# Kernel optimization log

Measured on AMD Instinct MI355X. Metric: run time of the kernel, lower is better.

Reference implementation:

```python
import jax, jax.numpy as jnp
import numpy as np

B, C_IN, C_INTER, H, W = 4, 256, 128, 64, 64


def _conv1x1(x, w, b):
    # x: [B,C,H,W], w: [O,C], b: [O] -> [B,O,H,W]
    return jnp.einsum('bchw,oc->bohw', x, w) + b[None, :, None, None]


def setup_inputs() -> dict:
    key = jax.random.key(0)
    ks = jax.random.split(key, 9)
    s_in = 1.0 / np.sqrt(C_IN)
    s_it = 1.0 / np.sqrt(C_INTER)
    return {
        'x': jax.random.normal(ks[0], (B, C_IN, H, W), dtype=jnp.float32),
        'theta_w': jax.random.normal(ks[1], (C_INTER, C_IN), dtype=jnp.float32) * s_in,
        'theta_b': jax.random.normal(ks[2], (C_INTER,), dtype=jnp.float32) * s_in,
        'phi_w': jax.random.normal(ks[3], (C_INTER, C_IN), dtype=jnp.float32) * s_in,
        'phi_b': jax.random.normal(ks[4], (C_INTER,), dtype=jnp.float32) * s_in,
        'g_w': jax.random.normal(ks[5], (C_INTER, C_IN), dtype=jnp.float32) * s_in,
        'g_b': jax.random.normal(ks[6], (C_INTER,), dtype=jnp.float32) * s_in,
        'W_w': jax.random.normal(ks[7], (C_IN, C_INTER), dtype=jnp.float32) * s_it,
        'W_b': jax.random.normal(ks[8], (C_IN,), dtype=jnp.float32) * s_it,
    }


def reference(x, theta_w, theta_b, phi_w, phi_b, g_w, g_b, W_w, W_b):
    b, c, h, w = x.shape
    n = h * w
    theta_x = _conv1x1(x, theta_w, theta_b).reshape(b, -1, n)  # [B,Ci,N]
    phi_x = _conv1x1(x, phi_w, phi_b).reshape(b, -1, n)        # [B,Ci,N]
    # f[b,i,j] = sum_c theta[b,c,i] * phi[b,c,j]  -> [B,N,N]
    f = jnp.einsum('bci,bcj->bij', theta_x, phi_x)
    # NOTE: softmax over dim=1 (the query/theta axis), as in the original code
    f_div_C = jax.nn.softmax(f, axis=1)
    g_x = _conv1x1(x, g_w, g_b).reshape(b, -1, n)              # [B,Ci,N]
    # y = f_div_C @ g_x^T, then permute back to [B,Ci,N] in one einsum
    y = jnp.einsum('bij,bcj->bci', f_div_C, g_x)
    y = y.reshape(b, -1, h, w)
    W_y = _conv1x1(y, W_w, W_b)
    return W_y + x
```

## Files before the change

kernel.cpp:

```cpp
#include <hip/hip_runtime.h>
#include <hip/hip_fp16.h>

#define NB   4
#define CIN  256
#define CM   128
#define NPIX 4096
#define LOG2E 1.44269504088896340736f

typedef _Float16 half_t;
typedef _Float16 f16x8 __attribute__((ext_vector_type(8)));
typedef _Float16 f16x4 __attribute__((ext_vector_type(4)));
typedef float    f32x4 __attribute__((ext_vector_type(4)));

static __device__ __forceinline__ f16x8 load8h(const half_t* p) {
    return *reinterpret_cast<const f16x8*>(p);
}
static __device__ __forceinline__ void gload_lds16(const void* g, void* l) {
    __builtin_amdgcn_global_load_lds(
        (const __attribute__((address_space(1))) unsigned int*)g,
        (__attribute__((address_space(3))) unsigned int*)l, 16, 0, 0);
}

__global__ __launch_bounds__(256) void k_pre(
    const float* __restrict__ tw, const float* __restrict__ pw,
    const float* __restrict__ gw, const float* __restrict__ Ww,
    half_t* __restrict__ TWh, half_t* __restrict__ PWh,
    half_t* __restrict__ GWh, half_t* __restrict__ WWh)
{
    const int m  = blockIdx.x >> 5;
    const int i4 = (blockIdx.x & 31) * 256 + threadIdx.x;
    const float* src = m == 0 ? tw : m == 1 ? pw : m == 2 ? gw : Ww;
    half_t*      dst = m == 0 ? TWh : m == 1 ? PWh : m == 2 ? GWh : WWh;
    float4 a = reinterpret_cast<const float4*>(src)[i4];
    f16x4 h = {(_Float16)a.x, (_Float16)a.y, (_Float16)a.z, (_Float16)a.w};
    *reinterpret_cast<f16x4*>(dst + (size_t)i4 * 4) = h;
}

__global__ __launch_bounds__(256) void k_proj(
    const float* __restrict__ x,
    const half_t* __restrict__ tw, const float* __restrict__ tb,
    const half_t* __restrict__ pw, const float* __restrict__ pb,
    const half_t* __restrict__ gw, const float* __restrict__ gb,
    half_t* __restrict__ T, half_t* __restrict__ P, half_t* __restrict__ G)
{
    __shared__ half_t xT[64][280];
    const int b  = blockIdx.x >> 6;
    const int p0 = (blockIdx.x & 63) << 6;
    const int tid = threadIdx.x;
    const int lane = tid & 63, wv = tid >> 6;
    const int r15 = lane & 15, g4 = lane >> 4;

    {
        const float* xb = x + (size_t)b * CIN * NPIX + p0;
        const int ii = tid & 63;
        const int k0 = tid >> 6;
        #pragma unroll 4
        for (int kk = 0; kk < 64; ++kk) {
            int k = kk * 4 + k0;
            xT[ii][k] = (half_t)xb[(size_t)k * NPIX + ii];
        }
    }
    __syncthreads();

    f16x8 afr[8];
    #pragma unroll
    for (int kg = 0; kg < 8; ++kg)
        afr[kg] = load8h(&xT[wv * 16 + r15][kg * 32 + g4 * 8]);

    #pragma unroll
    for (int p = 0; p < 2; ++p) {
        const half_t* wp = p ? pw : tw;
        const float*  bp = p ? pb : tb;
        half_t* OUT     = p ? P  : T;
        for (int cs = 0; cs < 8; ++cs) {
            f32x4 acc = {0.f, 0.f, 0.f, 0.f};
            const int crow = cs * 16 + r15;
            const half_t* wr = wp + (size_t)crow * CIN;
            #pragma unroll
            for (int kg = 0; kg < 8; ++kg) {
                f16x8 bf = load8h(wr + kg * 32 + g4 * 8);
                acc = __builtin_amdgcn_mfma_f32_16x16x32_f16(afr[kg], bf, acc, 0, 0, 0);
            }
            const float bias = bp[crow];
            #pragma unroll
            for (int r = 0; r < 4; ++r) {
                int pos = p0 + wv * 16 + g4 * 4 + r;
                OUT[((size_t)b * NPIX + pos) * CM + crow] = (half_t)(acc[r] + bias);
            }
        }
    }

    for (int cs = 0; cs < 8; ++cs) {
        f32x4 acc = {0.f, 0.f, 0.f, 0.f};
        const int crow = cs * 16 + r15;
        const half_t* wr = gw + (size_t)crow * CIN;
        #pragma unroll
        for (int kg = 0; kg < 8; ++kg) {
            f16x8 af = load8h(wr + kg * 32 + g4 * 8);
            acc = __builtin_amdgcn_mfma_f32_16x16x32_f16(af, afr[kg], acc, 0, 0, 0);
        }
        #pragma unroll
        for (int r = 0; r < 4; ++r) {
            int c = cs * 16 + g4 * 4 + r;
            int j = p0 + wv * 16 + r15;
            G[((size_t)b * CM + c) * NPIX + j] = (half_t)(acc[r] + gb[c]);
        }
    }
}

__global__ __launch_bounds__(512) void k_stats(
    const half_t* __restrict__ T, const half_t* __restrict__ P,
    float* __restrict__ M2, float* __restrict__ RD)
{
    __shared__ float partm[8][64];
    __shared__ float parts[8][64];
    const int b  = blockIdx.x >> 6;
    const int j0 = (blockIdx.x & 63) << 6;
    const int tid = threadIdx.x;
    const int lane = tid & 63, w = tid >> 6;
    const int r15 = lane & 15, g4 = lane >> 4;

    f16x8 bfr[4][4];
    const half_t* Pbase = P + (size_t)b * NPIX * CM;
    #pragma unroll
    for (int js = 0; js < 4; ++js)
        #pragma unroll
        for (int kg = 0; kg < 4; ++kg)
            bfr[js][kg] = load8h(Pbase + (size_t)(j0 + js * 16 + r15) * CM + kg * 32 + g4 * 8);

    float m2[4] = {-1e30f, -1e30f, -1e30f, -1e30f};
    float ss[4] = {0.f, 0.f, 0.f, 0.f};
    const half_t* Tb = T + (size_t)b * NPIX * CM;

    for (int it = 0; it < 8; ++it) {
        const int ibase = w * 512 + it * 64;
        #pragma unroll
        for (int is = 0; is < 4; ++is) {
            f16x8 af[4];
            const half_t* Tr = Tb + (size_t)(ibase + is * 16 + r15) * CM;
            #pragma unroll
            for (int kg = 0; kg < 4; ++kg) af[kg] = load8h(Tr + kg * 32 + g4 * 8);
            #pragma unroll
            for (int js = 0; js < 4; ++js) {
                f32x4 acc = {0.f, 0.f, 0.f, 0.f};
                #pragma unroll
                for (int kg = 0; kg < 4; ++kg)
                    acc = __builtin_amdgcn_mfma_f32_16x16x32_f16(af[kg], bfr[js][kg], acc, 0, 0, 0);
                float v0 = acc[0] * LOG2E, v1 = acc[1] * LOG2E;
                float v2 = acc[2] * LOG2E, v3 = acc[3] * LOG2E;
                float fm = fmaxf(fmaxf(v0, v1), fmaxf(v2, v3));
                float nm = fmaxf(m2[js], fm);
                ss[js] = ss[js] * exp2f(m2[js] - nm)
                       + (exp2f(v0 - nm) + exp2f(v1 - nm) + exp2f(v2 - nm) + exp2f(v3 - nm));
                m2[js] = nm;
            }
        }
    }
    #pragma unroll
    for (int js = 0; js < 4; ++js) {
        #pragma unroll
        for (int off = 16; off < 64; off <<= 1) {
            float om = __shfl_xor(m2[js], off);
            float os = __shfl_xor(ss[js], off);
            float nm = fmaxf(m2[js], om);
            ss[js] = ss[js] * exp2f(m2[js] - nm) + os * exp2f(om - nm);
            m2[js] = nm;
        }
        if (g4 == 0) { partm[w][js * 16 + r15] = m2[js]; parts[w][js * 16 + r15] = ss[js]; }
    }
    __syncthreads();
    if (tid < 64) {
        float m = -1e30f, s = 0.f;
        #pragma unroll
        for (int w2 = 0; w2 < 8; ++w2) {
            float om = partm[w2][tid], os = parts[w2][tid];
            float nm = fmaxf(m, om);
            s = s * exp2f(m - nm) + os * exp2f(om - nm);
            m = nm;
        }
        M2[b * NPIX + j0 + tid] = m;
        RD[b * NPIX + j0 + tid] = 1.0f / s;
    }
}

__global__ __launch_bounds__(256) void k_attn(
    const half_t* __restrict__ T, const half_t* __restrict__ P,
    const half_t* __restrict__ G,
    const float* __restrict__ M2, const float* __restrict__ RD,
    half_t* __restrict__ Y0, half_t* __restrict__ Y1)
{
    __shared__ half_t Pst[2][64 * 128];
    __shared__ half_t Gst[2][128 * 64];
    __shared__ half_t wlds[64][72];

    const int blk = blockIdx.x;
    const int b  = blk >> 7;
    const int ih = (blk >> 1) & 63;
    const int wg = blk & 1;
    const int i0 = ih << 6;
    const int tid = threadIdx.x;
    const int lane = tid & 63, wv = tid >> 6;
    const int r15 = lane & 15, g4 = lane >> 4;

    const half_t* Pb = P + (size_t)b * NPIX * CM;
    const half_t* Gb = G + (size_t)b * CM * NPIX;
    const float*  M2b = M2 + b * NPIX;
    const float*  RDb = RD + b * NPIX;

    f16x8 a1[4];
    const half_t* Tb = T + ((size_t)b * NPIX + i0 + wv * 16 + r15) * CM;
    #pragma unroll
    for (int kg = 0; kg < 4; ++kg) a1[kg] = load8h(Tb + kg * 32 + g4 * 8);

    f32x4 yacc[8];
    #pragma unroll
    for (int cs = 0; cs < 8; ++cs) yacc[cs] = (f32x4){0.f, 0.f, 0.f, 0.f};

    auto stageP = [&](int buf, int jb) {
        #pragma unroll
        for (int q = 0; q < 4; ++q) {
            int lo  = (wv * 4 + q) * 1024 + lane * 16;
            int row = lo >> 8;
            int cb  = lo & 255;
            const char* src = (const char*)Pb + (size_t)(jb + row) * (CM * 2)
                            + (cb ^ ((row & 7) << 4));
            gload_lds16(src, (char*)&Pst[buf][0] + (wv * 4 + q) * 1024);
        }
    };
    auto stageG = [&](int buf, int jb) {
        #pragma unroll
        for (int q = 0; q < 4; ++q) {
            int lo  = (wv * 4 + q) * 1024 + lane * 16;
            int row = lo >> 7;
            int cb  = lo & 127;
            const char* src = (const char*)Gb + (size_t)row * (NPIX * 2) + (size_t)jb * 2
                            + (cb ^ ((row & 7) << 4));
            gload_lds16(src, (char*)&Gst[buf][0] + (wv * 4 + q) * 1024);
        }
    };

    stageP(0, (wg * 32) * 64);
    stageG(0, (wg * 32) * 64);
    for (int jt = 0; jt < 32; ++jt) {
        const int jb = (wg * 32 + jt) * 64;
        const int cur = jt & 1;
        __syncthreads();
        if (jt < 31) { stageP(cur ^ 1, jb + 64); stageG(cur ^ 1, jb + 64); }

        const int swz = (r15 & 7) << 4;
        #pragma unroll
        for (int js = 0; js < 4; ++js) {
            f32x4 acc = {0.f, 0.f, 0.f, 0.f};
            const int row = js * 16 + r15;
            #pragma unroll
            for (int kg = 0; kg < 4; ++kg) {
                const char* pa = (const char*)&Pst[cur][0] + row * 256 + ((kg * 64 + g4 * 16) ^ swz);
                f16x8 bf = *reinterpret_cast<const f16x8*>(pa);
                acc = __builtin_amdgcn_mfma_f32_16x16x32_f16(a1[kg], bf, acc, 0, 0, 0);
            }
            const int j = jb + js * 16 + r15;
            const float mj = M2b[j], rdj = RDb[j];
            #pragma unroll
            for (int r = 0; r < 4; ++r) {
                float wgt = exp2f(fmaf(acc[r], LOG2E, -mj)) * rdj;
                wlds[wv * 16 + g4 * 4 + r][js * 16 + r15] = (half_t)wgt;
            }
        }

        f16x8 a2[2];
        #pragma unroll
        for (int kk = 0; kk < 2; ++kk)
            a2[kk] = load8h(&wlds[wv * 16 + r15][kk * 32 + g4 * 8]);
        #pragma unroll
        for (int cs = 0; cs < 8; ++cs) {
            const char* gbase = (const char*)&Gst[cur][0] + (cs * 16 + r15) * 128;
            #pragma unroll
            for (int kk = 0; kk < 2; ++kk) {
                f16x8 b2 = *reinterpret_cast<const f16x8*>(gbase + ((kk * 64 + g4 * 16) ^ swz));
                yacc[cs] = __builtin_amdgcn_mfma_f32_16x16x32_f16(a2[kk], b2, yacc[cs], 0, 0, 0);
            }
        }
    }

    half_t* Yp = wg ? Y1 : Y0;
    #pragma unroll
    for (int cs = 0; cs < 8; ++cs)
        #pragma unroll
        for (int r = 0; r < 4; ++r)
            Yp[((size_t)b * NPIX + i0 + wv * 16 + g4 * 4 + r) * CM + cs * 16 + r15]
                = (half_t)yacc[cs][r];
}

__global__ __launch_bounds__(256) void k_out(
    const half_t* __restrict__ Y0, const half_t* __restrict__ Y1,
    const half_t* __restrict__ Ww, const float* __restrict__ Wb,
    const float* __restrict__ x, float* __restrict__ out)
{
    const int b  = blockIdx.x >> 6;
    const int i0 = (blockIdx.x & 63) << 6;
    const int lane = threadIdx.x & 63, wv = threadIdx.x >> 6;
    const int r15 = lane & 15, g4 = lane >> 4;

    f16x8 yf[4];
    const size_t yrow = ((size_t)b * NPIX + i0 + wv * 16 + r15) * CM;
    #pragma unroll
    for (int kg = 0; kg < 4; ++kg) {
        f16x8 y0 = load8h(Y0 + yrow + kg * 32 + g4 * 8);
        f16x8 y1 = load8h(Y1 + yrow + kg * 32 + g4 * 8);
        yf[kg] = y0 + y1;
    }

    for (int os = 0; os < 16; ++os) {
        f32x4 acc = {0.f, 0.f, 0.f, 0.f};
        const half_t* wr = Ww + (size_t)(os * 16 + r15) * CM;
        #pragma unroll
        for (int kg = 0; kg < 4; ++kg) {
            f16x8 af = load8h(wr + kg * 32 + g4 * 8);
            acc = __builtin_amdgcn_mfma_f32_16x16x32_f16(af, yf[kg], acc, 0, 0, 0);
        }
        #pragma unroll
        for (int r = 0; r < 4; ++r) {
            int o = os * 16 + g4 * 4 + r;
            size_t addr = ((size_t)(b * CIN + o)) * NPIX + i0 + wv * 16 + r15;
            out[addr] = acc[r] + Wb[o] + x[addr];
        }
    }
}

extern "C" void kernel_launch(void* const* d_in, const int* in_sizes, int n_in,
                              void* d_out, int out_size, void* d_ws, size_t ws_size,
                              hipStream_t stream) {
    const float* x  = (const float*)d_in[0];
    const float* tw = (const float*)d_in[1];
    const float* tb = (const float*)d_in[2];
    const float* pw = (const float*)d_in[3];
    const float* pb = (const float*)d_in[4];
    const float* gw = (const float*)d_in[5];
    const float* gb = (const float*)d_in[6];
    const float* Ww = (const float*)d_in[7];
    const float* Wb = (const float*)d_in[8];
    float* out = (float*)d_out;

    const size_t SZ = (size_t)NB * NPIX * CM;
    const size_t WSZ = (size_t)CM * CIN;
    half_t* T   = (half_t*)d_ws;
    half_t* P   = T + SZ;
    half_t* G   = P + SZ;
    half_t* Y0  = G + SZ;
    half_t* Y1  = Y0 + SZ;
    half_t* TWh = Y1 + SZ;
    half_t* PWh = TWh + WSZ;
    half_t* GWh = PWh + WSZ;
    half_t* WWh = GWh + WSZ;
    float*  M2  = (float*)(WWh + WSZ);
    float*  RD  = M2 + (size_t)NB * NPIX;

    hipLaunchKernelGGL(k_pre,   dim3(128), dim3(256), 0, stream,
                       tw, pw, gw, Ww, TWh, PWh, GWh, WWh);
    hipLaunchKernelGGL(k_proj,  dim3(256), dim3(256), 0, stream,
                       x, TWh, tb, PWh, pb, GWh, gb, T, P, G);
    hipLaunchKernelGGL(k_stats, dim3(256), dim3(512), 0, stream, T, P, M2, RD);
    hipLaunchKernelGGL(k_attn,  dim3(512), dim3(256), 0, stream,
                       T, P, G, M2, RD, Y0, Y1);
    hipLaunchKernelGGL(k_out,   dim3(256), dim3(256), 0, stream,
                       Y0, Y1, WWh, Wb, x, out);
}
```

Before: 260.0 us.

## Split attention and stats work finer, drop weight LDS round-trip, fold softmax normalizer into logsumexp

Each k_stats block now covers 128 key columns and half of the query rows, writing partial max and sum values that a new k_merge kernel combines into one log-sum-exp per column. k_attn is split four ways along j (1024 blocks) and computes P·T with the operands swapped, so the exp weights land directly in the MFMA B-operand layout and feed 16x16x16 MFMAs without going through the wlds shared buffer. G is single-buffered with explicit vmcnt waits and a raw s_barrier, and the LSE values are loaded into LDS with an asynchronous 4-byte global-to-LDS load. The cost is four partial Y buffers to write and sum in k_out, an extra launch, and correctness that depends on hand-counted vmcnt values.

Result: slower. 271.6 us (+4.5%).

```diff
diff --git a/kernel.cpp b/kernel.cpp
--- a/kernel.cpp
+++ b/kernel.cpp
@@ -19,6 +19,11 @@
     __builtin_amdgcn_global_load_lds(
         (const __attribute__((address_space(1))) unsigned int*)g,
         (__attribute__((address_space(3))) unsigned int*)l, 16, 0, 0);
+}
+static __device__ __forceinline__ void gload_lds4(const void* g, void* l) {
+    __builtin_amdgcn_global_load_lds(
+        (const __attribute__((address_space(1))) unsigned int*)g,
+        (__attribute__((address_space(3))) unsigned int*)l, 4, 0, 0);
 }
 
 __global__ __launch_bounds__(256) void k_pre(
@@ -110,38 +115,41 @@
 
 __global__ __launch_bounds__(512) void k_stats(
     const half_t* __restrict__ T, const half_t* __restrict__ P,
-    float* __restrict__ M2, float* __restrict__ RD)
-{
-    __shared__ float partm[8][64];
-    __shared__ float parts[8][64];
+    float* __restrict__ Mp, float* __restrict__ Sp)
+{
+    __shared__ float partm[8][128];
+    __shared__ float parts[8][128];
     const int b  = blockIdx.x >> 6;
-    const int j0 = (blockIdx.x & 63) << 6;
+    const int jt = (blockIdx.x >> 1) & 31;
+    const int ih = blockIdx.x & 1;
+    const int j0 = jt * 128;
     const int tid = threadIdx.x;
     const int lane = tid & 63, w = tid >> 6;
     const int r15 = lane & 15, g4 = lane >> 4;
 
-    f16x8 bfr[4][4];
+    f16x8 bfr[8][4];
     const half_t* Pbase = P + (size_t)b * NPIX * CM;
     #pragma unroll
-    for (int js = 0; js < 4; ++js)
+    for (int js = 0; js < 8; ++js)
         #pragma unroll
         for (int kg = 0; kg < 4; ++kg)
             bfr[js][kg] = load8h(Pbase + (size_t)(j0 + js * 16 + r15) * CM + kg * 32 + g4 * 8);
 
-    float m2[4] = {-1e30f, -1e30f, -1e30f, -1e30f};
-    float ss[4] = {0.f, 0.f, 0.f, 0.f};
+    float m2[8], ss[8];
+    #pragma unroll
+    for (int js = 0; js < 8; ++js) { m2[js] = -1e30f; ss[js] = 0.f; }
     const half_t* Tb = T + (size_t)b * NPIX * CM;
-
-    for (int it = 0; it < 8; ++it) {
-        const int ibase = w * 512 + it * 64;
+    const int ibase0 = ih * 2048 + w * 256;
+
+    for (int it = 0; it < 4; ++it) {
         #pragma unroll
         for (int is = 0; is < 4; ++is) {
             f16x8 af[4];
-            const half_t* Tr = Tb + (size_t)(ibase + is * 16 + r15) * CM;
+            const half_t* Tr = Tb + (size_t)(ibase0 + it * 64 + is * 16 + r15) * CM;
             #pragma unroll
             for (int kg = 0; kg < 4; ++kg) af[kg] = load8h(Tr + kg * 32 + g4 * 8);
             #pragma unroll
-            for (int js = 0; js < 4; ++js) {
+            for (int js = 0; js < 8; ++js) {
                 f32x4 acc = {0.f, 0.f, 0.f, 0.f};
                 #pragma unroll
                 for (int kg = 0; kg < 4; ++kg)
@@ -157,7 +165,7 @@
         }
     }
     #pragma unroll
-    for (int js = 0; js < 4; ++js) {
+    for (int js = 0; js < 8; ++js) {
         #pragma unroll
         for (int off = 16; off < 64; off <<= 1) {
             float om = __shfl_xor(m2[js], off);
@@ -169,7 +177,7 @@
         if (g4 == 0) { partm[w][js * 16 + r15] = m2[js]; parts[w][js * 16 + r15] = ss[js]; }
     }
     __syncthreads();
-    if (tid < 64) {
+    if (tid < 128) {
         float m = -1e30f, s = 0.f;
         #pragma unroll
         for (int w2 = 0; w2 < 8; ++w2) {
@@ -178,34 +186,47 @@
             s = s * exp2f(m - nm) + os * exp2f(om - nm);
             m = nm;
         }
-        M2[b * NPIX + j0 + tid] = m;
-        RD[b * NPIX + j0 + tid] = 1.0f / s;
-    }
+        const size_t idx = (size_t)ih * (NB * NPIX) + b * NPIX + j0 + tid;
+        Mp[idx] = m;
+        Sp[idx] = s;
+    }
+}
+
+__global__ __launch_bounds__(256) void k_merge(
+    const float* __restrict__ Mp, const float* __restrict__ Sp,
+    float* __restrict__ C)
+{
+    const int idx = blockIdx.x * 256 + threadIdx.x;
+    const int nn = NB * NPIX;
+    float m0 = Mp[idx], m1 = Mp[nn + idx];
+    float s0 = Sp[idx], s1 = Sp[nn + idx];
+    float mm = fmaxf(m0, m1);
+    float s = s0 * exp2f(m0 - mm) + s1 * exp2f(m1 - mm);
+    C[idx] = mm + log2f(s);
 }
 
 __global__ __launch_bounds__(256) void k_attn(
     const half_t* __restrict__ T, const half_t* __restrict__ P,
-    const half_t* __restrict__ G,
-    const float* __restrict__ M2, const float* __restrict__ RD,
-    half_t* __restrict__ Y0, half_t* __restrict__ Y1)
+    const half_t* __restrict__ G, const float* __restrict__ C,
+    half_t* __restrict__ Y)
 {
     __shared__ half_t Pst[2][64 * 128];
-    __shared__ half_t Gst[2][128 * 64];
-    __shared__ half_t wlds[64][72];
+    __shared__ half_t Gst[128 * 64];
+    __shared__ float  Clds[64];
 
     const int blk = blockIdx.x;
-    const int b  = blk >> 7;
-    const int ih = (blk >> 1) & 63;
-    const int wg = blk & 1;
+    const int b  = blk >> 8;
+    const int ih = (blk >> 2) & 63;
+    const int jq = blk & 3;
     const int i0 = ih << 6;
+    const int jq0 = jq << 10;
     const int tid = threadIdx.x;
     const int lane = tid & 63, wv = tid >> 6;
     const int r15 = lane & 15, g4 = lane >> 4;
 
     const half_t* Pb = P + (size_t)b * NPIX * CM;
     const half_t* Gb = G + (size_t)b * CM * NPIX;
-    const float*  M2b = M2 + b * NPIX;
-    const float*  RDb = RD + b * NPIX;
+    const float*  Cb = C + b * NPIX;
 
     f16x8 a1[4];
     const half_t* Tb = T + ((size_t)b * NPIX + i0 + wv * 16 + r15) * CM;
@@ -227,7 +248,7 @@
             gload_lds16(src, (char*)&Pst[buf][0] + (wv * 4 + q) * 1024);
         }
     };
-    auto stageG = [&](int buf, int jb) {
+    auto stageG = [&](int jb) {
         #pragma unroll
         for (int q = 0; q < 4; ++q) {
             int lo  = (wv * 4 + q) * 1024 + lane * 16;
@@ -235,19 +256,25 @@
             int cb  = lo & 127;
             const char* src = (const char*)Gb + (size_t)row * (NPIX * 2) + (size_t)jb * 2
                             + (cb ^ ((row & 7) << 4));
-            gload_lds16(src, (char*)&Gst[buf][0] + (wv * 4 + q) * 1024);
+            gload_lds16(src, (char*)&Gst[0] + (wv * 4 + q) * 1024);
         }
     };
 
-    stageP(0, (wg * 32) * 64);
-    stageG(0, (wg * 32) * 64);
-    for (int jt = 0; jt < 32; ++jt) {
-        const int jb = (wg * 32 + jt) * 64;
+    stageP(0, jq0);
+    const int swz = (r15 & 7) << 4;
+
+    for (int jt = 0; jt < 16; ++jt) {
+        const int jb = jq0 + jt * 64;
         const int cur = jt & 1;
         __syncthreads();
-        if (jt < 31) { stageP(cur ^ 1, jb + 64); stageG(cur ^ 1, jb + 64); }
-
-        const int swz = (r15 & 7) << 4;
+
+        gload_lds4(Cb + jb + lane, &Clds[0]);
+        asm volatile("" ::: "memory");
+        stageG(jb);
+        asm volatile("" ::: "memory");
+        stageP(cur ^ 1, jt < 15 ? jb + 64 : jq0);
+
+        f32x4 facc[4];
         #pragma unroll
         for (int js = 0; js < 4; ++js) {
             f32x4 acc = {0.f, 0.f, 0.f, 0.f};
@@ -255,44 +282,51 @@
             #pragma unroll
             for (int kg = 0; kg < 4; ++kg) {
                 const char* pa = (const char*)&Pst[cur][0] + row * 256 + ((kg * 64 + g4 * 16) ^ swz);
-                f16x8 bf = *reinterpret_cast<const f16x8*>(pa);
-                acc = __builtin_amdgcn_mfma_f32_16x16x32_f16(a1[kg], bf, acc, 0, 0, 0);
+                f16x8 pf = *reinterpret_cast<const f16x8*>(pa);
+                acc = __builtin_amdgcn_mfma_f32_16x16x32_f16(pf, a1[kg], acc, 0, 0, 0);
             }
-            const int j = jb + js * 16 + r15;
-            const float mj = M2b[j], rdj = RDb[j];
-            #pragma unroll
-            for (int r = 0; r < 4; ++r) {
-                float wgt = exp2f(fmaf(acc[r], LOG2E, -mj)) * rdj;
-                wlds[wv * 16 + g4 * 4 + r][js * 16 + r15] = (half_t)wgt;
+            facc[js] = acc;
+        }
+
+        asm volatile("s_waitcnt vmcnt(8)" ::: "memory");
+
+        f16x4 wfrag[4];
+        #pragma unroll
+        for (int js = 0; js < 4; ++js) {
+            f32x4 cj = *reinterpret_cast<const f32x4*>(&Clds[js * 16 + g4 * 4]);
+            f16x4 wf;
+            #pragma unroll
+            for (int r = 0; r < 4; ++r)
+                wf[r] = (_Float16)exp2f(fmaf(facc[js][r], LOG2E, -cj[r]));
+            wfrag[js] = wf;
+        }
+
+        asm volatile("s_waitcnt vmcnt(4)" ::: "memory");
+        asm volatile("s_barrier" ::: "memory");
+
+        #pragma unroll
+        for (int cs = 0; cs < 8; ++cs) {
+            const char* gbase = (const char*)&Gst[0] + (cs * 16 + r15) * 128;
+            #pragma unroll
+            for (int js = 0; js < 4; ++js) {
+                f16x4 gf = *reinterpret_cast<const f16x4*>(gbase + ((js * 32 + g4 * 8) ^ swz));
+                yacc[cs] = __builtin_amdgcn_mfma_f32_16x16x16f16(gf, wfrag[js], yacc[cs], 0, 0, 0);
             }
         }
-
-        f16x8 a2[2];
-        #pragma unroll
-        for (int kk = 0; kk < 2; ++kk)
-            a2[kk] = load8h(&wlds[wv * 16 + r15][kk * 32 + g4 * 8]);
-        #pragma unroll
-        for (int cs = 0; cs < 8; ++cs) {
-            const char* gbase = (const char*)&Gst[cur][0] + (cs * 16 + r15) * 128;
-            #pragma unroll
-            for (int kk = 0; kk < 2; ++kk) {
-                f16x8 b2 = *reinterpret_cast<const f16x8*>(gbase + ((kk * 64 + g4 * 16) ^ swz));
-                yacc[cs] = __builtin_amdgcn_mfma_f32_16x16x32_f16(a2[kk], b2, yacc[cs], 0, 0, 0);
-            }
-        }
-    }
-
-    half_t* Yp = wg ? Y1 : Y0;
-    #pragma unroll
-    for (int cs = 0; cs < 8; ++cs)
-        #pragma unroll
-        for (int r = 0; r < 4; ++r)
-            Yp[((size_t)b * NPIX + i0 + wv * 16 + g4 * 4 + r) * CM + cs * 16 + r15]
-                = (half_t)yacc[cs][r];
+    }
+
+    half_t* Yq = Y + (size_t)jq * (NB * (size_t)NPIX * CM);
+    #pragma unroll
+    for (int cs = 0; cs < 8; ++cs) {
+        f16x4 yv = {(_Float16)yacc[cs][0], (_Float16)yacc[cs][1],
+                    (_Float16)yacc[cs][2], (_Float16)yacc[cs][3]};
+        *reinterpret_cast<f16x4*>(
+            Yq + ((size_t)b * NPIX + i0 + wv * 16 + r15) * CM + cs * 16 + g4 * 4) = yv;
+    }
 }
 
 __global__ __launch_bounds__(256) void k_out(
-    const half_t* __restrict__ Y0, const half_t* __restrict__ Y1,
+    const half_t* __restrict__ Y,
     const half_t* __restrict__ Ww, const float* __restrict__ Wb,
     const float* __restrict__ x, float* __restrict__ out)
 {
@@ -300,14 +334,17 @@
     const int i0 = (blockIdx.x & 63) << 6;
     const int lane = threadIdx.x & 63, wv = threadIdx.x >> 6;
     const int r15 = lane & 15, g4 = lane >> 4;
+    const size_t SZ = (size_t)NB * NPIX * CM;
 
     f16x8 yf[4];
     const size_t yrow = ((size_t)b * NPIX + i0 + wv * 16 + r15) * CM;
     #pragma unroll
     for (int kg = 0; kg < 4; ++kg) {
-        f16x8 y0 = load8h(Y0 + yrow + kg * 32 + g4 * 8);
-        f16x8 y1 = load8h(Y1 + yrow + kg * 32 + g4 * 8);
-        yf[kg] = y0 + y1;
+        f16x8 s0 = load8h(Y + yrow + kg * 32 + g4 * 8);
+        f16x8 s1 = load8h(Y + SZ + yrow + kg * 32 + g4 * 8);
+        f16x8 s2 = load8h(Y + 2 * SZ + yrow + kg * 32 + g4 * 8);
+        f16x8 s3 = load8h(Y + 3 * SZ + yrow + kg * 32 + g4 * 8);
+        yf[kg] = (s0 + s1) + (s2 + s3);
     }
 
     for (int os = 0; os < 16; ++os) {
@@ -341,27 +378,27 @@
     const float* Wb = (const float*)d_in[8];
     float* out = (float*)d_out;
 
-    const size_t SZ = (size_t)NB * NPIX * CM;
+    const size_t SZ  = (size_t)NB * NPIX * CM;
     const size_t WSZ = (size_t)CM * CIN;
+    const size_t NN  = (size_t)NB * NPIX;
     half_t* T   = (half_t*)d_ws;
     half_t* P   = T + SZ;
     half_t* G   = P + SZ;
-    half_t* Y0  = G + SZ;
-    half_t* Y1  = Y0 + SZ;
-    half_t* TWh = Y1 + SZ;
+    half_t* Y   = G + SZ;
+    half_t* TWh = Y + 4 * SZ;
     half_t* PWh = TWh + WSZ;
     half_t* GWh = PWh + WSZ;
     half_t* WWh = GWh + WSZ;
-    float*  M2  = (float*)(WWh + WSZ);
-    float*  RD  = M2 + (size_t)NB * NPIX;
-
-    hipLaunchKernelGGL(k_pre,   dim3(128), dim3(256), 0, stream,
+    float*  Mp  = (float*)(WWh + WSZ);
+    float*  Sp  = Mp + 2 * NN;
+    float*  C   = Sp + 2 * NN;
+
+    hipLaunchKernelGGL(k_pre,   dim3(128),  dim3(256), 0, stream,
                        tw, pw, gw, Ww, TWh, PWh, GWh, WWh);
-    hipLaunchKernelGGL(k_proj,  dim3(256), dim3(256), 0, stream,
+    hipLaunchKernelGGL(k_proj,  dim3(256),  dim3(256), 0, stream,
                        x, TWh, tb, PWh, pb, GWh, gb, T, P, G);
-    hipLaunchKernelGGL(k_stats, dim3(256), dim3(512), 0, stream, T, P, M2, RD);
-    hipLaunchKernelGGL(k_attn,  dim3(512), dim3(256), 0, stream,
-                       T, P, G, M2, RD, Y0, Y1);
-    hipLaunchKernelGGL(k_out,   dim3(256), dim3(256), 0, stream,
-                       Y0, Y1, WWh, Wb, x, out);
-}
+    hipLaunchKernelGGL(k_stats, dim3(256),  dim3(512), 0, stream, T, P, Mp, Sp);
+    hipLaunchKernelGGL(k_merge, dim3(64),   dim3(256), 0, stream, Mp, Sp, C);
+    hipLaunchKernelGGL(k_attn,  dim3(1024), dim3(256), 0, stream, T, P, G, C, Y);
+    hipLaunchKernelGGL(k_out,   dim3(256),  dim3(256), 0, stream, Y, WWh, Wb, x, out);
+}
```
